# Optimization experiments

Measured on AMD Instinct MI355X. Metric: run time of the kernel, lower is better.

## Reference

```python
import jax, jax.numpy as jnp
import numpy as np

N_NODES = 50000
N_EDGES = 800000
IN_DIM, HID_DIM, OUT_DIM = 256, 128, 64


def setup_inputs() -> dict:
    key = jax.random.key(0)
    ks = jax.random.split(key, 8)
    x = jax.random.normal(ks[0], (N_NODES, IN_DIM), dtype=jnp.float32)
    edge_index = jax.random.randint(ks[1], (2, N_EDGES), 0, N_NODES, dtype=jnp.int64)
    # Glorot-ish init for GCNConv weights (PyG stores weight as [in, out] in lin layer; math is x @ W)
    def glorot(k, shape):
        lim = (6.0 / (shape[0] + shape[1])) ** 0.5
        return jax.random.uniform(k, shape, jnp.float32, -lim, lim)
    return {
        "x": x,
        "edge_index": edge_index,
        "W1": glorot(ks[2], (IN_DIM, HID_DIM)), "b1": jnp.zeros((HID_DIM,), jnp.float32),
        "W2": glorot(ks[3], (HID_DIM, HID_DIM)), "b2": jnp.zeros((HID_DIM,), jnp.float32),
        "W3": glorot(ks[4], (HID_DIM, OUT_DIM)), "b3": jnp.zeros((OUT_DIM,), jnp.float32),
    }


def _gcn_norm(edge_index, n):
    # PyG gcn_norm with add_self_loops=True: A_hat = D^-1/2 (A + I) D^-1/2
    loops = jnp.arange(n, dtype=edge_index.dtype)
    src = jnp.concatenate([edge_index[0], loops])  # [E+N]
    dst = jnp.concatenate([edge_index[1], loops])  # [E+N]
    deg = jax.ops.segment_sum(jnp.ones_like(dst, dtype=jnp.float32), dst, num_segments=n)
    dinv = jnp.where(deg > 0, deg ** -0.5, 0.0)
    norm = dinv[src] * dinv[dst]  # [E+N]
    return src, dst, norm


def _gcn_layer(x, W, b, src, dst, norm, n):
    h = x @ W                                  # [N, F_out] transform first (GCNConv order)
    m = h[src] * norm[:, None]                 # edge-gather + normalize
    agg = jax.ops.segment_sum(m, dst, num_segments=n)  # scatter-add aggregation
    return agg + b


def reference(x, edge_index, W1, b1, W2, b2, W3, b3):
    n = x.shape[0]
    src, dst, norm = _gcn_norm(edge_index, n)
    h = jax.nn.relu(_gcn_layer(x, W1, b1, src, dst, norm, n))
    h = jax.nn.relu(_gcn_layer(h, W2, b2, src, dst, norm, n))
    h = jax.nn.relu(_gcn_layer(h, W3, b3, src, dst, norm, n))
    return h
```

## Files before the change

kernel.cpp:

```cpp
#include <hip/hip_runtime.h>
#include <math.h>

typedef _Float16 half8v __attribute__((ext_vector_type(8)));
typedef float    f32x4  __attribute__((ext_vector_type(4)));

#define DSTR 16


__global__ void wcvt_zero_kernel(const float* __restrict__ W1, _Float16* __restrict__ Bt1,
                                 const float* __restrict__ W2, _Float16* __restrict__ Bt2,
                                 const float* __restrict__ W3, _Float16* __restrict__ Bt3,
                                 int* __restrict__ deg, int n) {
    int i = blockIdx.x * blockDim.x + threadIdx.x;
    if (i < n) deg[(size_t)i * DSTR] = 0;
    if (i < 256 * 128) {
        int k = i & 255, nn = i >> 8;
        Bt1[i] = (_Float16)W1[(size_t)k * 128 + nn];
    } else if (i < 256 * 128 + 128 * 128) {
        int j = i - 256 * 128;
        int k = j & 127, nn = j >> 7;
        Bt2[j] = (_Float16)W2[(size_t)k * 128 + nn];
    } else if (i < 256 * 128 + 128 * 128 + 128 * 64) {
        int j = i - 256 * 128 - 128 * 128;
        int k = j & 127, nn = j >> 7;
        Bt3[j] = (_Float16)W3[(size_t)k * 64 + nn];
    }
}

__global__ void deg_pos_kernel(const int* __restrict__ dst, int* __restrict__ deg,
                               int* __restrict__ pos, int E) {
    int i = blockIdx.x * blockDim.x + threadIdx.x;
    if (i < E) pos[i] = atomicAdd(&deg[(size_t)dst[i] * DSTR], 1);
}

__global__ __launch_bounds__(256) void scan1_kernel(const int* __restrict__ deg,
                                                    int* __restrict__ row_ptr,
                                                    int* __restrict__ partial,
                                                    float* __restrict__ dinv, int n) {
    __shared__ int s[256];
    int tid = threadIdx.x;
    int i = blockIdx.x * 256 + tid;
    int dg = (i < n) ? deg[(size_t)i * DSTR] : 0;
    if (i < n) dinv[i] = 1.0f / sqrtf((float)(dg + 1));
    int v = (i < n) ? ((dg + 4) & ~3) : 0;
    s[tid] = v;
    __syncthreads();
    #pragma unroll
    for (int off = 1; off < 256; off <<= 1) {
        int t = (tid >= off) ? s[tid - off] : 0;
        __syncthreads();
        s[tid] += t;
        __syncthreads();
    }
    if (i < n) row_ptr[i + 1] = s[tid];
    if (tid == 255) partial[blockIdx.x] = s[255];
}

__global__ __launch_bounds__(256) void scan2_kernel(int* __restrict__ partial, int nb) {
    __shared__ int s[256];
    int tid = threadIdx.x;
    int v = (tid < nb) ? partial[tid] : 0;
    s[tid] = v;
    __syncthreads();
    #pragma unroll
    for (int off = 1; off < 256; off <<= 1) {
        int t = (tid >= off) ? s[tid - off] : 0;
        __syncthreads();
        s[tid] += t;
        __syncthreads();
    }
    if (tid < nb) partial[tid] = s[tid] - v;
}

__global__ void scan3_kernel(const int* __restrict__ partial, int* __restrict__ row_ptr, int n) {
    int i = blockIdx.x * blockDim.x + threadIdx.x;
    if (i == 0) row_ptr[0] = 0;
    if (i < n) row_ptr[i + 1] += partial[i >> 8];
}

__device__ __forceinline__ void fill_body(int bid,
                            const int* __restrict__ ei, const int* __restrict__ pos,
                            const int* __restrict__ deg, const float* __restrict__ dinv,
                            const int* __restrict__ row_ptr, unsigned* __restrict__ csr,
                            int E, int n) {
    int idx = bid * 256 + threadIdx.x;
    int s, d, slot;
    if (idx < E)          { s = ei[idx]; d = ei[E + idx]; slot = pos[idx]; }
    else if (idx < E + n) { s = d = idx - E; slot = deg[(size_t)d * DSTR]; }
    else if (idx < E + n + 3 * n) {
        int p = idx - E - n;
        int dd = p / 3, pi = p - dd * 3;
        int dg = deg[(size_t)dd * DSTR];
        int real = dg + 1;
        int padded = (dg + 4) & ~3;
        if (pi < padded - real) csr[row_ptr[dd] + real + pi] = 0u;
        return;
    } else return;
    float w = dinv[s] * dinv[d];
    union { _Float16 h; unsigned short u; } cv; cv.h = (_Float16)w;
    csr[row_ptr[d] + slot] = (unsigned)s | ((unsigned)cv.u << 16);
}

template <typename TA, int K, int TNv>
__device__ __forceinline__ void gemm_body(int bid, const TA* __restrict__ A,
                                          const _Float16* __restrict__ Bt,
                                          _Float16* __restrict__ C, int M) {
    constexpr int NF = TNv / 16;
    constexpr int KP = K + 8;
    constexpr int CHUNKS = (TNv * (K / 8)) / 256;
    __shared__ _Float16 Bs[TNv * KP];

    int tid = threadIdx.x;
    #pragma unroll
    for (int i = 0; i < CHUNKS; ++i) {
        int id = tid + i * 256;
        int n  = id / (K / 8);
        int k8 = (id % (K / 8)) * 8;
        *(half8v*)(&Bs[n * KP + k8]) = *(const half8v*)(Bt + (size_t)n * K + k8);
    }
    __syncthreads();

    int lane = tid & 63;
    int wave = tid >> 6;
    int r  = lane & 15;
    int kg = lane >> 4;
    int row0 = bid * 128 + wave * 32;

    f32x4 acc[2][NF];
    #pragma unroll
    for (int mf = 0; mf < 2; ++mf)
        #pragma unroll
        for (int nf = 0; nf < NF; ++nf)
            acc[mf][nf] = (f32x4){0.f, 0.f, 0.f, 0.f};

    int rowA0 = row0 + r;      if (rowA0 > M - 1) rowA0 = M - 1;
    int rowA1 = row0 + 16 + r; if (rowA1 > M - 1) rowA1 = M - 1;
    const TA* pa0 = A + (size_t)rowA0 * K + kg * 8;
    const TA* pa1 = A + (size_t)rowA1 * K + kg * 8;

    #pragma unroll
    for (int kc = 0; kc < K; kc += 32) {
        half8v a0, a1;
        if constexpr (__is_same(TA, float)) {
            float4 l0 = *(const float4*)(pa0 + kc);
            float4 h0 = *(const float4*)(pa0 + kc + 4);
            float4 l1 = *(const float4*)(pa1 + kc);
            float4 h1 = *(const float4*)(pa1 + kc + 4);
            a0[0] = (_Float16)l0.x; a0[1] = (_Float16)l0.y; a0[2] = (_Float16)l0.z; a0[3] = (_Float16)l0.w;
            a0[4] = (_Float16)h0.x; a0[5] = (_Float16)h0.y; a0[6] = (_Float16)h0.z; a0[7] = (_Float16)h0.w;
            a1[0] = (_Float16)l1.x; a1[1] = (_Float16)l1.y; a1[2] = (_Float16)l1.z; a1[3] = (_Float16)l1.w;
            a1[4] = (_Float16)h1.x; a1[5] = (_Float16)h1.y; a1[6] = (_Float16)h1.z; a1[7] = (_Float16)h1.w;
        } else {
            a0 = *(const half8v*)(pa0 + kc);
            a1 = *(const half8v*)(pa1 + kc);
        }
        #pragma unroll
        for (int nf = 0; nf < NF; ++nf) {
            half8v b = *(const half8v*)(&Bs[(nf * 16 + r) * KP + kc + kg * 8]);
            acc[0][nf] = __builtin_amdgcn_mfma_f32_16x16x32_f16(a0, b, acc[0][nf], 0, 0, 0);
            acc[1][nf] = __builtin_amdgcn_mfma_f32_16x16x32_f16(a1, b, acc[1][nf], 0, 0, 0);
        }
    }

    #pragma unroll
    for (int mf = 0; mf < 2; ++mf) {
        #pragma unroll
        for (int j = 0; j < 4; ++j) {
            int row = row0 + mf * 16 + kg * 4 + j;
            if (row < M) {
                #pragma unroll
                for (int nf = 0; nf < NF; ++nf)
                    C[(size_t)row * TNv + nf * 16 + r] = (_Float16)acc[mf][nf][j];
            }
        }
    }
}

template <typename TA, int K, int TNv>
__global__ __launch_bounds__(256) void mfma_gemm_kernel(const TA* __restrict__ A,
                                                        const _Float16* __restrict__ Bt,
                                                        _Float16* __restrict__ C,
                                                        int M) {
    gemm_body<TA, K, TNv>(blockIdx.x, A, Bt, C, M);
}

__global__ __launch_bounds__(256) void fill_gemm1_kernel(
    const int* __restrict__ ei, const int* __restrict__ pos,
    const int* __restrict__ deg, const float* __restrict__ dinv,
    const int* __restrict__ row_ptr, unsigned* __restrict__ csr, int E, int n,
    const float* __restrict__ A, const _Float16* __restrict__ Bt,
    _Float16* __restrict__ C, int M, int gemm_blocks)
{
    if (blockIdx.x < gemm_blocks)
        gemm_body<float, 256, 128>(blockIdx.x, A, Bt, C, M);
    else
        fill_body(blockIdx.x - gemm_blocks, ei, pos, deg, dinv, row_ptr, csr, E, n);
}

template <int F, typename TOut>
__global__ __launch_bounds__(256) void spmm_kernel(const _Float16* __restrict__ H,
                                                   const int* __restrict__ row_ptr,
                                                   const unsigned* __restrict__ csr,
                                                   const float* __restrict__ bias,
                                                   TOut* __restrict__ out,
                                                   int n_nodes) {
    constexpr int LPR = F / 8;
    constexpr int RPW = 64 / LPR;
    constexpr int U16 = 16 / RPW;
    constexpr int U8  = 8 / RPW;
    int wave = threadIdx.x >> 6;
    int lane = threadIdx.x & 63;
    int node = (blockIdx.x << 2) + wave;
    if (node >= n_nodes) return;

    int h  = lane / LPR;
    int fi = (lane % LPR) * 8;
    const _Float16* Hf = H + fi;

    int e0 = row_ptr[node];
    int e1 = row_ptr[node + 1];

    float acc[U16][8];
    #pragma unroll
    for (int i = 0; i < U16; ++i)
        #pragma unroll
        for (int j = 0; j < 8; ++j) acc[i][j] = 0.f;

    auto unpack_w = [](unsigned pk) -> float {
        union { unsigned short u; _Float16 h; } cv;
        cv.u = (unsigned short)(pk >> 16);
        return (float)cv.h;
    };

    int e = e0;
    for (; e + 16 <= e1; e += 16) {
        unsigned pk[U16];
        #pragma unroll
        for (int i = 0; i < U16; ++i) pk[i] = csr[e + i * RPW + h];
        #pragma unroll
        for (int i = 0; i < U16; ++i) {
            half8v v = *(const half8v*)(Hf + (size_t)(pk[i] & 0xFFFFu) * F);
            float w = unpack_w(pk[i]);
            #pragma unroll
            for (int j = 0; j < 8; ++j) acc[i][j] = fmaf(w, (float)v[j], acc[i][j]);
        }
    }
    if (e + 8 <= e1) {
        unsigned pk[U8];
        #pragma unroll
        for (int i = 0; i < U8; ++i) pk[i] = csr[e + i * RPW + h];
        #pragma unroll
        for (int i = 0; i < U8; ++i) {
            half8v v = *(const half8v*)(Hf + (size_t)(pk[i] & 0xFFFFu) * F);
            float w = unpack_w(pk[i]);
            #pragma unroll
            for (int j = 0; j < 8; ++j) acc[i][j] = fmaf(w, (float)v[j], acc[i][j]);
        }
        e += 8;
    }
    if (e < e1) {
        unsigned pk = (RPW == 4 || h < 4) ? csr[e + h] : 0u;
        half8v v = *(const half8v*)(Hf + (size_t)(pk & 0xFFFFu) * F);
        float w = unpack_w(pk);
        #pragma unroll
        for (int j = 0; j < 8; ++j) acc[0][j] = fmaf(w, (float)v[j], acc[0][j]);
    }

    float t[8];
    #pragma unroll
    for (int j = 0; j < 8; ++j) {
        t[j] = acc[0][j];
        #pragma unroll
        for (int i = 1; i < U16; ++i) t[j] += acc[i][j];
    }
    #pragma unroll
    for (int off = LPR; off < 64; off <<= 1)
        #pragma unroll
        for (int j = 0; j < 8; ++j) t[j] += __shfl_xor(t[j], off);

    if (h == 0) {
        float4 bl = *(const float4*)(bias + fi);
        float4 bh = *(const float4*)(bias + fi + 4);
        float o[8];
        o[0] = fmaxf(t[0] + bl.x, 0.f); o[1] = fmaxf(t[1] + bl.y, 0.f);
        o[2] = fmaxf(t[2] + bl.z, 0.f); o[3] = fmaxf(t[3] + bl.w, 0.f);
        o[4] = fmaxf(t[4] + bh.x, 0.f); o[5] = fmaxf(t[5] + bh.y, 0.f);
        o[6] = fmaxf(t[6] + bh.z, 0.f); o[7] = fmaxf(t[7] + bh.w, 0.f);
        if constexpr (__is_same(TOut, _Float16)) {
            half8v hv;
            #pragma unroll
            for (int j = 0; j < 8; ++j) hv[j] = (_Float16)o[j];
            *(half8v*)(out + (size_t)node * F + fi) = hv;
        } else {
            *(float4*)(out + (size_t)node * F + fi)     = make_float4(o[0], o[1], o[2], o[3]);
            *(float4*)(out + (size_t)node * F + fi + 4) = make_float4(o[4], o[5], o[6], o[7]);
        }
    }
}


extern "C" void kernel_launch(void* const* d_in, const int* in_sizes, int n_in,
                              void* d_out, int out_size, void* d_ws, size_t ws_size,
                              hipStream_t stream) {
    const float* x  = (const float*)d_in[0];
    const int*   ei = (const int*)d_in[1];
    const float* W1 = (const float*)d_in[2];
    const float* b1 = (const float*)d_in[3];
    const float* W2 = (const float*)d_in[4];
    const float* b2 = (const float*)d_in[5];
    const float* W3 = (const float*)d_in[6];
    const float* b3 = (const float*)d_in[7];

    const int IN_DIM = 256, HID = 128, OUT = 64;
    int n_nodes = in_sizes[0] / IN_DIM;
    int n_edges = in_sizes[1] / 2;
    int nnz_cap = n_edges + 4 * n_nodes;

    char* ws = (char*)d_ws;
    size_t off = 0;
    auto carve = [&](size_t bytes) { void* p = ws + off; off += (bytes + 255) & ~(size_t)255; return p; };
    _Float16* Hbuf = (_Float16*)carve((size_t)n_nodes * HID * sizeof(_Float16));
    _Float16* Bbuf = (_Float16*)carve((size_t)n_nodes * HID * sizeof(_Float16));
    _Float16* Bt1  = (_Float16*)carve((size_t)IN_DIM * HID * sizeof(_Float16));
    _Float16* Bt2  = (_Float16*)carve((size_t)HID * HID * sizeof(_Float16));
    _Float16* Bt3  = (_Float16*)carve((size_t)HID * OUT * sizeof(_Float16));
    int*   deg     = (int*)carve((size_t)n_nodes * DSTR * sizeof(int));
    float* dinv    = (float*)carve((size_t)n_nodes * sizeof(float));
    int*   row_ptr = (int*)carve((size_t)(n_nodes + 1) * sizeof(int));
    int*   pos     = (int*)carve((size_t)n_edges * sizeof(int));
    int*   partial = (int*)carve(256 * sizeof(int));
    unsigned* csr  = (unsigned*)carve((size_t)nnz_cap * sizeof(unsigned));
    if (off > ws_size) return;

    float* out = (float*)d_out;

    const int B = 256;
    int nb = (n_nodes + 255) / 256;
    int wtot = IN_DIM * HID + HID * HID + HID * OUT;

    wcvt_zero_kernel<<<(wtot + B - 1) / B, B, 0, stream>>>(W1, Bt1, W2, Bt2, W3, Bt3,
                                                           deg, n_nodes);
    deg_pos_kernel<<<(n_edges + B - 1) / B, B, 0, stream>>>(ei + n_edges, deg, pos, n_edges);
    scan1_kernel<<<nb, 256, 0, stream>>>(deg, row_ptr, partial, dinv, n_nodes);
    scan2_kernel<<<1, 256, 0, stream>>>(partial, nb);
    scan3_kernel<<<(n_nodes + B - 1) / B, B, 0, stream>>>(partial, row_ptr, n_nodes);

    int spmm_grid = (n_nodes + 3) / 4;
    int gemm_grid = (n_nodes + 127) / 128;
    int fill_grid = (n_edges + 4 * n_nodes + B - 1) / B;

    fill_gemm1_kernel<<<gemm_grid + fill_grid, 256, 0, stream>>>(
        ei, pos, deg, dinv, row_ptr, csr, n_edges, n_nodes,
        x, Bt1, Hbuf, n_nodes, gemm_grid);

    spmm_kernel<128, _Float16><<<spmm_grid, 256, 0, stream>>>(Hbuf, row_ptr, csr, b1, Bbuf, n_nodes);
    mfma_gemm_kernel<_Float16, 128, 128><<<gemm_grid, 256, 0, stream>>>(Bbuf, Bt2, Hbuf, n_nodes);
    spmm_kernel<128, _Float16><<<spmm_grid, 256, 0, stream>>>(Hbuf, row_ptr, csr, b2, Bbuf, n_nodes);
    mfma_gemm_kernel<_Float16, 128, 64><<<gemm_grid, 256, 0, stream>>>(Bbuf, Bt3, Hbuf, n_nodes);
    spmm_kernel<64, float><<<spmm_grid, 256, 0, stream>>>(Hbuf, row_ptr, csr, b3, out, n_nodes);
}
```

Baseline: 184.4 us.

## Drop scan3 pass by folding block offsets into row_ptr reads; register-resident gemm1

Removes the scan3 kernel launch and instead adds the per-block scan offset on the fly wherever row_ptr is read (fill and the three spmm kernels). The fused fill+gemm1 kernel also gets a new GEMM body: each block now computes 32 rows, each wave owns a 32-column slice, and W1 is held in registers instead of being staged through LDS. This gives more, smaller GEMM blocks. The cost is an extra partial[] load per row_ptr access and more register pressure in gemm1.

```diff
diff --git a/kernel.cpp b/kernel.cpp
--- a/kernel.cpp
+++ b/kernel.cpp
@@ -72,17 +72,16 @@
     if (tid < nb) partial[tid] = s[tid] - v;
 }
 
-__global__ void scan3_kernel(const int* __restrict__ partial, int* __restrict__ row_ptr, int n) {
-    int i = blockIdx.x * blockDim.x + threadIdx.x;
-    if (i == 0) row_ptr[0] = 0;
-    if (i < n) row_ptr[i + 1] += partial[i >> 8];
+__device__ __forceinline__ int rp_final(const int* __restrict__ row_ptr,
+                                        const int* __restrict__ partial, int j) {
+    return (j == 0) ? 0 : row_ptr[j] + partial[(j - 1) >> 8];
 }
 
 __device__ __forceinline__ void fill_body(int bid,
                             const int* __restrict__ ei, const int* __restrict__ pos,
                             const int* __restrict__ deg, const float* __restrict__ dinv,
-                            const int* __restrict__ row_ptr, unsigned* __restrict__ csr,
-                            int E, int n) {
+                            const int* __restrict__ row_ptr, const int* __restrict__ partial,
+                            unsigned* __restrict__ csr, int E, int n) {
     int idx = bid * 256 + threadIdx.x;
     int s, d, slot;
     if (idx < E)          { s = ei[idx]; d = ei[E + idx]; slot = pos[idx]; }
@@ -93,18 +92,95 @@
         int dg = deg[(size_t)dd * DSTR];
         int real = dg + 1;
         int padded = (dg + 4) & ~3;
-        if (pi < padded - real) csr[row_ptr[dd] + real + pi] = 0u;
+        if (pi < padded - real)
+            csr[rp_final(row_ptr, partial, dd) + real + pi] = 0u;
         return;
     } else return;
     float w = dinv[s] * dinv[d];
     union { _Float16 h; unsigned short u; } cv; cv.h = (_Float16)w;
-    csr[row_ptr[d] + slot] = (unsigned)s | ((unsigned)cv.u << 16);
+    csr[rp_final(row_ptr, partial, d) + slot] = (unsigned)s | ((unsigned)cv.u << 16);
+}
+
+__device__ __forceinline__ void gemm1_reg_body(int bid, const float* __restrict__ A,
+                                               const _Float16* __restrict__ Bt,
+                                               _Float16* __restrict__ C, int M) {
+    int tid = threadIdx.x;
+    int lane = tid & 63;
+    int wave = tid >> 6;
+    int r  = lane & 15;
+    int kg = lane >> 4;
+    int row0 = bid * 32;
+    int col0 = wave * 32;
+
+    half8v b[2][8];
+    #pragma unroll
+    for (int nf = 0; nf < 2; ++nf)
+        #pragma unroll
+        for (int kc = 0; kc < 8; ++kc)
+            b[nf][kc] = *(const half8v*)(Bt + (size_t)(col0 + nf * 16 + r) * 256 + kc * 32 + kg * 8);
+
+    f32x4 acc[2][2];
+    #pragma unroll
+    for (int mf = 0; mf < 2; ++mf)
+        #pragma unroll
+        for (int nf = 0; nf < 2; ++nf)
+            acc[mf][nf] = (f32x4){0.f, 0.f, 0.f, 0.f};
+
+    int rowA0 = row0 + r;      if (rowA0 > M - 1) rowA0 = M - 1;
+    int rowA1 = row0 + 16 + r; if (rowA1 > M - 1) rowA1 = M - 1;
+    const float* pa0 = A + (size_t)rowA0 * 256 + kg * 8;
+    const float* pa1 = A + (size_t)rowA1 * 256 + kg * 8;
+
+    #pragma unroll
+    for (int kc = 0; kc < 8; ++kc) {
+        float4 l0 = *(const float4*)(pa0 + kc * 32);
+        float4 h0 = *(const float4*)(pa0 + kc * 32 + 4);
+        float4 l1 = *(const float4*)(pa1 + kc * 32);
+        float4 h1 = *(const float4*)(pa1 + kc * 32 + 4);
+        half8v a0, a1;
+        a0[0] = (_Float16)l0.x; a0[1] = (_Float16)l0.y; a0[2] = (_Float16)l0.z; a0[3] = (_Float16)l0.w;
+        a0[4] = (_Float16)h0.x; a0[5] = (_Float16)h0.y; a0[6] = (_Float16)h0.z; a0[7] = (_Float16)h0.w;
+        a1[0] = (_Float16)l1.x; a1[1] = (_Float16)l1.y; a1[2] = (_Float16)l1.z; a1[3] = (_Float16)l1.w;
+        a1[4] = (_Float16)h1.x; a1[5] = (_Float16)h1.y; a1[6] = (_Float16)h1.z; a1[7] = (_Float16)h1.w;
+        acc[0][0] = __builtin_amdgcn_mfma_f32_16x16x32_f16(a0, b[0][kc], acc[0][0], 0, 0, 0);
+        acc[0][1] = __builtin_amdgcn_mfma_f32_16x16x32_f16(a0, b[1][kc], acc[0][1], 0, 0, 0);
+        acc[1][0] = __builtin_amdgcn_mfma_f32_16x16x32_f16(a1, b[0][kc], acc[1][0], 0, 0, 0);
+        acc[1][1] = __builtin_amdgcn_mfma_f32_16x16x32_f16(a1, b[1][kc], acc[1][1], 0, 0, 0);
+    }
+
+    #pragma unroll
+    for (int mf = 0; mf < 2; ++mf) {
+        #pragma unroll
+        for (int j = 0; j < 4; ++j) {
+            int row = row0 + mf * 16 + kg * 4 + j;
+            if (row < M) {
+                #pragma unroll
+                for (int nf = 0; nf < 2; ++nf)
+                    C[(size_t)row * 128 + col0 + nf * 16 + r] = (_Float16)acc[mf][nf][j];
+            }
+        }
+    }
+}
+
+__global__ __launch_bounds__(256) void fill_gemm1_kernel(
+    const int* __restrict__ ei, const int* __restrict__ pos,
+    const int* __restrict__ deg, const float* __restrict__ dinv,
+    const int* __restrict__ row_ptr, const int* __restrict__ partial,
+    unsigned* __restrict__ csr, int E, int n,
+    const float* __restrict__ A, const _Float16* __restrict__ Bt,
+    _Float16* __restrict__ C, int M, int gemm_blocks)
+{
+    if (blockIdx.x < gemm_blocks)
+        gemm1_reg_body(blockIdx.x, A, Bt, C, M);
+    else
+        fill_body(blockIdx.x - gemm_blocks, ei, pos, deg, dinv, row_ptr, partial, csr, E, n);
 }
 
 template <typename TA, int K, int TNv>
-__device__ __forceinline__ void gemm_body(int bid, const TA* __restrict__ A,
-                                          const _Float16* __restrict__ Bt,
-                                          _Float16* __restrict__ C, int M) {
+__global__ __launch_bounds__(256) void mfma_gemm_kernel(const TA* __restrict__ A,
+                                                        const _Float16* __restrict__ Bt,
+                                                        _Float16* __restrict__ C,
+                                                        int M) {
     constexpr int NF = TNv / 16;
     constexpr int KP = K + 8;
     constexpr int CHUNKS = (TNv * (K / 8)) / 256;
@@ -124,7 +200,7 @@
     int wave = tid >> 6;
     int r  = lane & 15;
     int kg = lane >> 4;
-    int row0 = bid * 128 + wave * 32;
+    int row0 = blockIdx.x * 128 + wave * 32;
 
     f32x4 acc[2][NF];
     #pragma unroll
@@ -140,20 +216,8 @@
 
     #pragma unroll
     for (int kc = 0; kc < K; kc += 32) {
-        half8v a0, a1;
-        if constexpr (__is_same(TA, float)) {
-            float4 l0 = *(const float4*)(pa0 + kc);
-            float4 h0 = *(const float4*)(pa0 + kc + 4);
-            float4 l1 = *(const float4*)(pa1 + kc);
-            float4 h1 = *(const float4*)(pa1 + kc + 4);
-            a0[0] = (_Float16)l0.x; a0[1] = (_Float16)l0.y; a0[2] = (_Float16)l0.z; a0[3] = (_Float16)l0.w;
-            a0[4] = (_Float16)h0.x; a0[5] = (_Float16)h0.y; a0[6] = (_Float16)h0.z; a0[7] = (_Float16)h0.w;
-            a1[0] = (_Float16)l1.x; a1[1] = (_Float16)l1.y; a1[2] = (_Float16)l1.z; a1[3] = (_Float16)l1.w;
-            a1[4] = (_Float16)h1.x; a1[5] = (_Float16)h1.y; a1[6] = (_Float16)h1.z; a1[7] = (_Float16)h1.w;
-        } else {
-            a0 = *(const half8v*)(pa0 + kc);
-            a1 = *(const half8v*)(pa1 + kc);
-        }
+        half8v a0 = *(const half8v*)(pa0 + kc);
+        half8v a1 = *(const half8v*)(pa1 + kc);
         #pragma unroll
         for (int nf = 0; nf < NF; ++nf) {
             half8v b = *(const half8v*)(&Bs[(nf * 16 + r) * KP + kc + kg * 8]);
@@ -176,30 +240,10 @@
     }
 }
 
-template <typename TA, int K, int TNv>
-__global__ __launch_bounds__(256) void mfma_gemm_kernel(const TA* __restrict__ A,
-                                                        const _Float16* __restrict__ Bt,
-                                                        _Float16* __restrict__ C,
-                                                        int M) {
-    gemm_body<TA, K, TNv>(blockIdx.x, A, Bt, C, M);
-}
-
-__global__ __launch_bounds__(256) void fill_gemm1_kernel(
-    const int* __restrict__ ei, const int* __restrict__ pos,
-    const int* __restrict__ deg, const float* __restrict__ dinv,
-    const int* __restrict__ row_ptr, unsigned* __restrict__ csr, int E, int n,
-    const float* __restrict__ A, const _Float16* __restrict__ Bt,
-    _Float16* __restrict__ C, int M, int gemm_blocks)
-{
-    if (blockIdx.x < gemm_blocks)
-        gemm_body<float, 256, 128>(blockIdx.x, A, Bt, C, M);
-    else
-        fill_body(blockIdx.x - gemm_blocks, ei, pos, deg, dinv, row_ptr, csr, E, n);
-}
-
 template <int F, typename TOut>
 __global__ __launch_bounds__(256) void spmm_kernel(const _Float16* __restrict__ H,
                                                    const int* __restrict__ row_ptr,
+                                                   const int* __restrict__ partial,
                                                    const unsigned* __restrict__ csr,
                                                    const float* __restrict__ bias,
                                                    TOut* __restrict__ out,
@@ -217,8 +261,8 @@
     int fi = (lane % LPR) * 8;
     const _Float16* Hf = H + fi;
 
-    int e0 = row_ptr[node];
-    int e1 = row_ptr[node + 1];
+    int e0 = rp_final(row_ptr, partial, node);
+    int e1 = rp_final(row_ptr, partial, node + 1);
 
     float acc[U16][8];
     #pragma unroll
@@ -343,19 +387,19 @@
     deg_pos_kernel<<<(n_edges + B - 1) / B, B, 0, stream>>>(ei + n_edges, deg, pos, n_edges);
     scan1_kernel<<<nb, 256, 0, stream>>>(deg, row_ptr, partial, dinv, n_nodes);
     scan2_kernel<<<1, 256, 0, stream>>>(partial, nb);
-    scan3_kernel<<<(n_nodes + B - 1) / B, B, 0, stream>>>(partial, row_ptr, n_nodes);
-
-    int spmm_grid = (n_nodes + 3) / 4;
-    int gemm_grid = (n_nodes + 127) / 128;
-    int fill_grid = (n_edges + 4 * n_nodes + B - 1) / B;
-
-    fill_gemm1_kernel<<<gemm_grid + fill_grid, 256, 0, stream>>>(
-        ei, pos, deg, dinv, row_ptr, csr, n_edges, n_nodes,
-        x, Bt1, Hbuf, n_nodes, gemm_grid);
-
-    spmm_kernel<128, _Float16><<<spmm_grid, 256, 0, stream>>>(Hbuf, row_ptr, csr, b1, Bbuf, n_nodes);
+
+    int spmm_grid  = (n_nodes + 3) / 4;
+    int gemm_grid  = (n_nodes + 127) / 128;
+    int gemm1_grid = (n_nodes + 31) / 32;
+    int fill_grid  = (n_edges + 4 * n_nodes + B - 1) / B;
+
+    fill_gemm1_kernel<<<gemm1_grid + fill_grid, 256, 0, stream>>>(
+        ei, pos, deg, dinv, row_ptr, partial, csr, n_edges, n_nodes,
+        x, Bt1, Hbuf, n_nodes, gemm1_grid);
+
+    spmm_kernel<128, _Float16><<<spmm_grid, 256, 0, stream>>>(Hbuf, row_ptr, partial, csr, b1, Bbuf, n_nodes);
     mfma_gemm_kernel<_Float16, 128, 128><<<gemm_grid, 256, 0, stream>>>(Bbuf, Bt2, Hbuf, n_nodes);
-    spmm_kernel<128, _Float16><<<spmm_grid, 256, 0, stream>>>(Hbuf, row_ptr, csr, b2, Bbuf, n_nodes);
+    spmm_kernel<128, _Float16><<<spmm_grid, 256, 0, stream>>>(Hbuf, row_ptr, partial, csr, b2, Bbuf, n_nodes);
     mfma_gemm_kernel<_Float16, 128, 64><<<gemm_grid, 256, 0, stream>>>(Bbuf, Bt3, Hbuf, n_nodes);
-    spmm_kernel<64, float><<<spmm_grid, 256, 0, stream>>>(Hbuf, row_ptr, csr, b3, out, n_nodes);
-}
+    spmm_kernel<64, float><<<spmm_grid, 256, 0, stream>>>(Hbuf, row_ptr, partial, csr, b3, out, n_nodes);
+}
```

New measurement: 210.8 us. 14.3% more time.
